# Kernel optimization log

Measured on AMD Instinct MI355X. Metric: run time of the kernel, lower is better.

The kernel has to match this reference:

```python
import jax, jax.numpy as jnp
import numpy as np

DIM = 64
H = 4
POS_DIM = 4
NUM_IDS = 16
B = 2048
N = 64


def setup_inputs() -> dict:
    key = jax.random.key(0)
    ks = jax.random.split(key, 16)
    d8 = DIM // 8
    stdv = 1.0 / np.sqrt(DIM * DIM)
    inp = {
        "x": jax.random.normal(ks[0], (B, N, DIM), jnp.float32),
        "pos": jax.random.normal(ks[1], (B, N, POS_DIM), jnp.float32),
        "strength": jax.random.normal(ks[2], (512,), jnp.float32),
        "embed_id1": 3,
        # weights stored [in, out] (torch Linear weight transposed)
        "Wq": jax.random.normal(ks[3], (DIM, DIM), jnp.float32) * 0.05,
        "Wk": jax.random.normal(ks[4], (DIM, DIM), jnp.float32) * 0.05,
        "pos_W1": jax.random.normal(ks[5], (POS_DIM, POS_DIM), jnp.float32) * 0.3,
        "pos_b1": jnp.zeros((POS_DIM,), jnp.float32),
        "pos_W2": jax.random.normal(ks[6], (POS_DIM, d8), jnp.float32) * 0.3,
        "pos_b2": jnp.zeros((d8,), jnp.float32),
        "head_W": jax.random.normal(ks[7], (d8, H), jnp.float32) * 0.3,
        "head_b": jnp.zeros((H,), jnp.float32),
        "gate": jnp.ones((H,), jnp.float32),
        "embeds": jax.random.uniform(ks[8], (NUM_IDS, DIM * DIM), jnp.float32, -stdv, stdv),
        "out_W": jax.random.normal(ks[9], (DIM, DIM), jnp.float32) * 0.05,
        "out_b": jnp.zeros((DIM,), jnp.float32),
        "str_W": jax.random.normal(ks[10], (512, 64), jnp.float32) * 0.04,
        "str_b": jnp.zeros((64,), jnp.float32),
    }
    return inp


def reference(x, pos, strength, embed_id1, Wq, Wk, pos_W1, pos_b1, pos_W2, pos_b2,
              head_W, head_b, gate, embeds, out_W, out_b, str_W, str_b):
    Bb, Nn, dim = x.shape
    h = gate.shape[0]
    dh = dim // h

    # strength projection, added to dynamic-weight V
    s64 = strength @ str_W + str_b                       # [dim]
    E = embeds[embed_id1].reshape(dim, dim)              # per-sample V weight
    v = x @ E.T + s64                                    # F.linear(x, E) + strength
    v = v.reshape(Bb, Nn, h, dh).transpose(0, 2, 1, 3)   # [B,H,N,dh]

    # QK attention
    q = (x @ Wq).reshape(Bb, Nn, h, dh).transpose(0, 2, 1, 3)
    k = (x @ Wk).reshape(Bb, Nn, h, dh).transpose(0, 2, 1, 3)
    attn = jax.nn.softmax(jnp.einsum('bhqd,bhkd->bhqk', q, k) / np.sqrt(dh), axis=-1)

    # pairwise relative-position attention
    p = jax.nn.relu(pos @ pos_W1 + pos_b1) @ pos_W2 + pos_b2          # [B,N,dim//8]
    diff = p[:, :, None, :] - p[:, None, :, :]                        # [B,N,N,dim//8]
    pos_logits = jnp.einsum('bqkf,fh->bhqk', diff, head_W) + head_b[None, :, None, None]
    pos_attn = jax.nn.softmax(pos_logits, axis=-1)

    # sigmoid-gated mixing + renormalization
    g = jax.nn.sigmoid(gate)[None, :, None, None]
    attn = (1.0 - g) * attn + g * pos_attn
    attn = attn / jnp.sum(attn, axis=-1, keepdims=True)

    out = jnp.einsum('bhqk,bhkd->bhqd', attn, v)
    out = out.transpose(0, 2, 1, 3).reshape(Bb, Nn, dim)
    return out @ out_W + out_b
```

## Files before the change

### kernel.cpp

```cpp
#include <hip/hip_runtime.h>

typedef unsigned short u16;
typedef unsigned int u32;
typedef short bf8 __attribute__((ext_vector_type(8)));
typedef float f4v __attribute__((ext_vector_type(4)));
typedef float f16v __attribute__((ext_vector_type(16)));

#define STR 72

__device__ __forceinline__ u32 f2bf(float f){
    union{float f;u32 i;}c; c.f=f; u32 i=c.i;
    return (i + 0x7FFFu + ((i>>16)&1u)) >> 16;
}

__device__ __forceinline__ void stage_row16(const float* __restrict__ g, short* __restrict__ dst,
                                            int n, int c0){
    const float4* p = (const float4*)(g + n*64 + c0);
    float4 a=p[0], b=p[1], c=p[2], d=p[3];
    uint4 o0, o1;
    o0.x = f2bf(a.x)|(f2bf(a.y)<<16); o0.y = f2bf(a.z)|(f2bf(a.w)<<16);
    o0.z = f2bf(b.x)|(f2bf(b.y)<<16); o0.w = f2bf(b.z)|(f2bf(b.w)<<16);
    o1.x = f2bf(c.x)|(f2bf(c.y)<<16); o1.y = f2bf(c.z)|(f2bf(c.w)<<16);
    o1.z = f2bf(d.x)|(f2bf(d.y)<<16); o1.w = f2bf(d.z)|(f2bf(d.w)<<16);
    *(uint4*)&dst[n*STR + c0]     = o0;
    *(uint4*)&dst[n*STR + c0 + 8] = o1;
}

__device__ __forceinline__ void mmgB(const u16* __restrict__ Wt, bf8 a0, bf8 a1,
                                     int l15, int quad, f4v c[4]){
    #pragma unroll
    for (int nt=0; nt<4; ++nt){
        bf8 b0 = *(const bf8*)&Wt[(16*nt + l15)*64 + quad*8];
        bf8 b1 = *(const bf8*)&Wt[(16*nt + l15)*64 + 32 + quad*8];
        c[nt] = __builtin_amdgcn_mfma_f32_16x16x32_bf16(a0, b0, c[nt], 0,0,0);
        c[nt] = __builtin_amdgcn_mfma_f32_16x16x32_bf16(a1, b1, c[nt], 0,0,0);
    }
}

__global__ __launch_bounds__(256) void pre_kernel(
    const int* __restrict__ embed_id,
    const float* __restrict__ Wq, const float* __restrict__ Wk, const float* __restrict__ oW,
    const float* __restrict__ embeds, const float* __restrict__ sW, const float* __restrict__ sb,
    const float* __restrict__ strength,
    float* __restrict__ ws_s64, u16* __restrict__ ws_wq, u16* __restrict__ ws_wk,
    u16* __restrict__ ws_ow, u16* __restrict__ ws_e)
{
    const int j = blockIdx.x;
    const int t = threadIdx.x;

    if (j < 3) {
        const float* W = (j==0) ? Wq : (j==1) ? Wk : oW;
        u16* dst = (j==0) ? ws_wq : (j==1) ? ws_wk : ws_ow;
        const int kp = t >> 3, ng = t & 7;
        const float4* r0 = (const float4*)(W + (2*kp  )*64 + 8*ng);
        const float4* r1 = (const float4*)(W + (2*kp+1)*64 + 8*ng);
        float4 a0=r0[0], a1=r0[1], b0=r1[0], b1=r1[1];
        float lo[8]={a0.x,a0.y,a0.z,a0.w,a1.x,a1.y,a1.z,a1.w};
        float hi[8]={b0.x,b0.y,b0.z,b0.w,b1.x,b1.y,b1.z,b1.w};
        #pragma unroll
        for (int i=0;i<8;++i)
            *(u32*)&dst[(8*ng+i)*64 + 2*kp] = f2bf(lo[i]) | (f2bf(hi[i])<<16);
    } else {
        __shared__ float sp[4][64];
        {
            const int n = t >> 2, c0 = (t & 3) << 4;
            const float4* p = (const float4*)(embeds + (size_t)(*embed_id)*4096 + n*64 + c0);
            float4 a=p[0], b=p[1], c=p[2], d=p[3];
            uint4 o0, o1;
            o0.x = f2bf(a.x)|(f2bf(a.y)<<16); o0.y = f2bf(a.z)|(f2bf(a.w)<<16);
            o0.z = f2bf(b.x)|(f2bf(b.y)<<16); o0.w = f2bf(b.z)|(f2bf(b.w)<<16);
            o1.x = f2bf(c.x)|(f2bf(c.y)<<16); o1.y = f2bf(c.z)|(f2bf(c.w)<<16);
            o1.z = f2bf(d.x)|(f2bf(d.y)<<16); o1.w = f2bf(d.z)|(f2bf(d.w)<<16);
            *(uint4*)&ws_e[n*64 + c0]     = o0;
            *(uint4*)&ws_e[n*64 + c0 + 8] = o1;
        }
        {
            const int d = t & 63, part = t >> 6;
            const float* wp = sW + part*128*64 + d;
            const float* s  = strength + part*128;
            float acc = 0.f;
            #pragma unroll 8
            for (int i = 0; i < 128; ++i) acc = fmaf(s[i], wp[i*64], acc);
            sp[part][d] = acc;
        }
        __syncthreads();
        if (t < 64) ws_s64[t] = sp[0][t] + sp[1][t] + sp[2][t] + sp[3][t] + sb[t];
    }
}

__global__ __launch_bounds__(256, 3) void attn_main_kernel(
    const float* __restrict__ x, const float* __restrict__ pos,
    const float* __restrict__ gate, const float* __restrict__ ob,
    const float* __restrict__ pW1, const float* __restrict__ pb1,
    const float* __restrict__ pW2, const float* __restrict__ pb2,
    const float* __restrict__ hW,
    const float* __restrict__ ws_s64,
    const u16* __restrict__ ws_wq, const u16* __restrict__ ws_wk,
    const u16* __restrict__ ws_ow, const u16* __restrict__ ws_e,
    float* __restrict__ out)
{
    __shared__ short B0[64*STR];
    __shared__ short B1[64*STR];
    __shared__ short B2[64*STR];
    __shared__ short B3[64*STR];
    __shared__ short VT[64*STR];
    __shared__ float pat_l[4][64];

    const int t    = threadIdx.x;
    const int b    = blockIdx.x;
    const int lane = t & 63;
    const int w    = t >> 6;
    const int l15  = lane & 15;
    const int l31  = lane & 31;
    const int l5   = lane >> 5;
    const int quad = lane >> 4;
    const int n    = t >> 2;
    const int c0   = (t & 3) << 4;

    stage_row16(x + (size_t)b*4096, B0, n, c0);

    float g = 1.f/(1.f + __expf(-gate[w]));
    {
        const float4 pv = *(const float4*)(pos + ((size_t)b*64 + lane)*4);
        float h1[4], p8[8];
        #pragma unroll
        for (int jj = 0; jj < 4; ++jj){
            float a = pb1[jj];
            a = fmaf(pv.x, pW1[0*4+jj], a);
            a = fmaf(pv.y, pW1[1*4+jj], a);
            a = fmaf(pv.z, pW1[2*4+jj], a);
            a = fmaf(pv.w, pW1[3*4+jj], a);
            h1[jj] = fmaxf(a, 0.f);
        }
        #pragma unroll
        for (int f = 0; f < 8; ++f){
            float a = pb2[f];
            #pragma unroll
            for (int jj = 0; jj < 4; ++jj) a = fmaf(h1[jj], pW2[jj*8+f], a);
            p8[f] = a;
        }
        float tv = 0.f;
        #pragma unroll
        for (int f = 0; f < 8; ++f) tv = fmaf(p8[f], hW[f*4+w], tv);
        float v0 = -tv;
        float m = v0;
        #pragma unroll
        for (int off = 32; off; off >>= 1) m = fmaxf(m, __shfl_xor(m, off));
        float e = __expf(v0 - m);
        float ssum = e;
        #pragma unroll
        for (int off = 32; off; off >>= 1) ssum += __shfl_xor(ssum, off);
        pat_l[w][lane] = g * (e / ssum);
    }

    float svv[4];
    #pragma unroll
    for (int nt=0;nt<4;++nt) svv[nt] = ws_s64[16*nt + l15];
    float obv[4];
    #pragma unroll
    for (int nt=0;nt<4;++nt) obv[nt] = ob[16*nt + l15];

    asm volatile("" ::: "memory");

    {
        bf8 xa0 = *(const bf8*)&B0[(16*w + l15)*STR + quad*8];
        bf8 xa1 = *(const bf8*)&B0[(16*w + l15)*STR + 32 + quad*8];
        f4v cq[4], ck[4], cv[4];
        #pragma unroll
        for (int nt=0;nt<4;++nt){
            cq[nt][0]=0.f;cq[nt][1]=0.f;cq[nt][2]=0.f;cq[nt][3]=0.f;
            ck[nt][0]=0.f;ck[nt][1]=0.f;ck[nt][2]=0.f;ck[nt][3]=0.f;
            cv[nt][0]=0.f;cv[nt][1]=0.f;cv[nt][2]=0.f;cv[nt][3]=0.f;
        }
        mmgB(ws_wq, xa0, xa1, l15, quad, cq);
        mmgB(ws_wk, xa0, xa1, l15, quad, ck);
        mmgB(ws_e,  xa0, xa1, l15, quad, cv);
        #pragma unroll
        for (int nt=0;nt<4;++nt)
            #pragma unroll
            for (int r=0;r<4;++r){
                B2[(16*w + quad*4 + r)*STR + 16*nt + l15] = (short)f2bf(0.25f*cq[nt][r]);
                B3[(16*w + quad*4 + r)*STR + 16*nt + l15] = (short)f2bf(ck[nt][r]);
            }
        #pragma unroll
        for (int nt=0;nt<4;++nt){
            float sv = svv[nt];
            uint2 pk;
            pk.x = f2bf(cv[nt][0]+sv) | (f2bf(cv[nt][1]+sv)<<16);
            pk.y = f2bf(cv[nt][2]+sv) | (f2bf(cv[nt][3]+sv)<<16);
            *(uint2*)&VT[(16*nt + l15)*STR + 16*w + quad*4] = pk;
        }
    }
    __syncthreads();

    f16v S[2][2];
    {
        bf8 ka0 = *(const bf8*)&B3[(     l31)*STR + 16*w + 8*l5];
        bf8 ka1 = *(const bf8*)&B3[(32 + l31)*STR + 16*w + 8*l5];
        bf8 qb0 = *(const bf8*)&B2[(     l31)*STR + 16*w + 8*l5];
        bf8 qb1 = *(const bf8*)&B2[(32 + l31)*STR + 16*w + 8*l5];
        #pragma unroll
        for (int mt=0;mt<2;++mt)
            #pragma unroll
            for (int nt=0;nt<2;++nt)
                #pragma unroll
                for (int i=0;i<16;++i) S[mt][nt][i] = 0.f;
        S[0][0] = __builtin_amdgcn_mfma_f32_32x32x16_bf16(ka0, qb0, S[0][0], 0,0,0);
        S[0][1] = __builtin_amdgcn_mfma_f32_32x32x16_bf16(ka0, qb1, S[0][1], 0,0,0);
        S[1][0] = __builtin_amdgcn_mfma_f32_32x32x16_bf16(ka1, qb0, S[1][0], 0,0,0);
        S[1][1] = __builtin_amdgcn_mfma_f32_32x32x16_bf16(ka1, qb1, S[1][1], 0,0,0);
    }
    float inv_[2];
    #pragma unroll
    for (int nt=0;nt<2;++nt){
        float m = S[0][nt][0];
        #pragma unroll
        for (int i=1;i<16;++i) m = fmaxf(m, S[0][nt][i]);
        #pragma unroll
        for (int i=0;i<16;++i) m = fmaxf(m, S[1][nt][i]);
        m = fmaxf(m, __shfl_xor(m, 32));
        float l = 0.f;
        #pragma unroll
        for (int mt=0;mt<2;++mt)
            #pragma unroll
            for (int i=0;i<16;++i){ float e = __expf(S[mt][nt][i]-m); S[mt][nt][i] = e; l += e; }
        l += __shfl_xor(l, 32);
        float c1 = (1.f - g) / l;
        float tot = 0.f;
        #pragma unroll
        for (int mt=0;mt<2;++mt)
            #pragma unroll
            for (int rg=0;rg<4;++rg){
                const float4 tv = *(const float4*)&pat_l[w][32*mt + 8*rg + 4*l5];
                float a0 = fmaf(c1, S[mt][nt][rg*4+0], tv.x);
                float a1 = fmaf(c1, S[mt][nt][rg*4+1], tv.y);
                float a2 = fmaf(c1, S[mt][nt][rg*4+2], tv.z);
                float a3 = fmaf(c1, S[mt][nt][rg*4+3], tv.w);
                S[mt][nt][rg*4+0]=a0; S[mt][nt][rg*4+1]=a1;
                S[mt][nt][rg*4+2]=a2; S[mt][nt][rg*4+3]=a3;
                tot += a0+a1+a2+a3;
            }
        tot += __shfl_xor(tot, 32);
        inv_[nt] = 1.f / tot;
    }
    __syncthreads();

    short* Pb = (w==0) ? B0 : (w==1) ? B1 : (w==2) ? B2 : B3;
    #pragma unroll
    for (int nt=0;nt<2;++nt)
        #pragma unroll
        for (int mt=0;mt<2;++mt)
            #pragma unroll
            for (int rg=0;rg<4;++rg){
                float v0 = S[mt][nt][rg*4+0]*inv_[nt], v1 = S[mt][nt][rg*4+1]*inv_[nt];
                float v2 = S[mt][nt][rg*4+2]*inv_[nt], v3 = S[mt][nt][rg*4+3]*inv_[nt];
                uint2 pk;
                pk.x = f2bf(v0) | (f2bf(v1)<<16);
                pk.y = f2bf(v2) | (f2bf(v3)<<16);
                *(uint2*)&Pb[(32*nt + l31)*STR + 32*mt + 8*rg + 4*l5] = pk;
            }
    asm volatile("" ::: "memory");

    f4v o[4];
    {
        bf8 bv0 = *(const bf8*)&VT[(16*w + l15)*STR + quad*8];
        bf8 bv1 = *(const bf8*)&VT[(16*w + l15)*STR + 32 + quad*8];
        #pragma unroll
        for (int mt=0;mt<4;++mt){
            o[mt][0]=0.f;o[mt][1]=0.f;o[mt][2]=0.f;o[mt][3]=0.f;
            bf8 a0 = *(const bf8*)&Pb[(16*mt + l15)*STR + quad*8];
            bf8 a1 = *(const bf8*)&Pb[(16*mt + l15)*STR + 32 + quad*8];
            o[mt] = __builtin_amdgcn_mfma_f32_16x16x32_bf16(a0, bv0, o[mt], 0,0,0);
            o[mt] = __builtin_amdgcn_mfma_f32_16x16x32_bf16(a1, bv1, o[mt], 0,0,0);
        }
    }
    __syncthreads();

    #pragma unroll
    for (int mt=0;mt<4;++mt)
        #pragma unroll
        for (int r=0;r<4;++r)
            B3[(16*mt + quad*4 + r)*STR + 16*w + l15] = (short)f2bf(o[mt][r]);
    __syncthreads();

    {
        bf8 ca0 = *(const bf8*)&B3[(16*w + l15)*STR + quad*8];
        bf8 ca1 = *(const bf8*)&B3[(16*w + l15)*STR + 32 + quad*8];
        f4v c[4];
        #pragma unroll
        for (int nt=0;nt<4;++nt){
            c[nt][0]=obv[nt];c[nt][1]=obv[nt];c[nt][2]=obv[nt];c[nt][3]=obv[nt];
        }
        mmgB(ws_ow, ca0, ca1, l15, quad, c);
        #pragma unroll
        for (int nt=0;nt<4;++nt)
            #pragma unroll
            for (int r=0;r<4;++r)
                out[((size_t)b*64 + 16*w + quad*4 + r)*64 + 16*nt + l15] = c[nt][r];
    }
}

extern "C" void kernel_launch(void* const* d_in, const int* in_sizes, int n_in,
                              void* d_out, int out_size, void* d_ws, size_t ws_size,
                              hipStream_t stream) {
    const int B = in_sizes[0] / (64 * 64);

    float* ws_s64 = (float*)d_ws;
    u16*   ws_wq  = (u16*)(ws_s64 + 64);
    u16*   ws_wk  = ws_wq + 4096;
    u16*   ws_ow  = ws_wk + 4096;
    u16*   ws_e   = ws_ow + 4096;

    pre_kernel<<<4, 256, 0, stream>>>(
        (const int*)d_in[3],
        (const float*)d_in[4],  (const float*)d_in[5],  (const float*)d_in[14],
        (const float*)d_in[13], (const float*)d_in[16], (const float*)d_in[17],
        (const float*)d_in[2],
        ws_s64, ws_wq, ws_wk, ws_ow, ws_e);

    attn_main_kernel<<<B, 256, 0, stream>>>(
        (const float*)d_in[0],  (const float*)d_in[1],
        (const float*)d_in[12], (const float*)d_in[15],
        (const float*)d_in[6],  (const float*)d_in[7],  (const float*)d_in[8],  (const float*)d_in[9],
        (const float*)d_in[10],
        ws_s64, ws_wq, ws_wk, ws_ow, ws_e,
        (float*)d_out);
}
```

Baseline: 153.5 us.

## Split projection GEMMs by output column so weight fragments stay in registers

```diff
diff --git a/kernel.cpp b/kernel.cpp
--- a/kernel.cpp
+++ b/kernel.cpp
@@ -26,17 +26,6 @@
     *(uint4*)&dst[n*STR + c0 + 8] = o1;
 }
 
-__device__ __forceinline__ void mmgB(const u16* __restrict__ Wt, bf8 a0, bf8 a1,
-                                     int l15, int quad, f4v c[4]){
-    #pragma unroll
-    for (int nt=0; nt<4; ++nt){
-        bf8 b0 = *(const bf8*)&Wt[(16*nt + l15)*64 + quad*8];
-        bf8 b1 = *(const bf8*)&Wt[(16*nt + l15)*64 + 32 + quad*8];
-        c[nt] = __builtin_amdgcn_mfma_f32_16x16x32_bf16(a0, b0, c[nt], 0,0,0);
-        c[nt] = __builtin_amdgcn_mfma_f32_16x16x32_bf16(a1, b1, c[nt], 0,0,0);
-    }
-}
-
 __global__ __launch_bounds__(256) void pre_kernel(
     const int* __restrict__ embed_id,
     const float* __restrict__ Wq, const float* __restrict__ Wk, const float* __restrict__ oW,
@@ -51,6 +40,7 @@
     if (j < 3) {
         const float* W = (j==0) ? Wq : (j==1) ? Wk : oW;
         u16* dst = (j==0) ? ws_wq : (j==1) ? ws_wk : ws_ow;
+        const float scl = (j==0) ? 0.25f : 1.0f;
         const int kp = t >> 3, ng = t & 7;
         const float4* r0 = (const float4*)(W + (2*kp  )*64 + 8*ng);
         const float4* r1 = (const float4*)(W + (2*kp+1)*64 + 8*ng);
@@ -59,7 +49,7 @@
         float hi[8]={b0.x,b0.y,b0.z,b0.w,b1.x,b1.y,b1.z,b1.w};
         #pragma unroll
         for (int i=0;i<8;++i)
-            *(u32*)&dst[(8*ng+i)*64 + 2*kp] = f2bf(lo[i]) | (f2bf(hi[i])<<16);
+            *(u32*)&dst[(8*ng+i)*64 + 2*kp] = f2bf(scl*lo[i]) | (f2bf(scl*hi[i])<<16);
     } else {
         __shared__ float sp[4][64];
         {
@@ -100,7 +90,7 @@
     float* __restrict__ out)
 {
     __shared__ short B0[64*STR];
-    __shared__ short B1[64*STR];
+    __shared__ short PX[64*STR];
     __shared__ short B2[64*STR];
     __shared__ short B3[64*STR];
     __shared__ short VT[64*STR];
@@ -117,6 +107,18 @@
     const int n    = t >> 2;
     const int c0   = (t & 3) << 4;
 
+    const int wq_off = (16*w + l15)*64 + quad*8;
+    bf8 bq0 = *(const bf8*)&ws_wq[wq_off];
+    bf8 bq1 = *(const bf8*)&ws_wq[wq_off + 32];
+    bf8 bk0 = *(const bf8*)&ws_wk[wq_off];
+    bf8 bk1 = *(const bf8*)&ws_wk[wq_off + 32];
+    bf8 be0 = *(const bf8*)&ws_e [wq_off];
+    bf8 be1 = *(const bf8*)&ws_e [wq_off + 32];
+    bf8 bo0 = *(const bf8*)&ws_ow[wq_off];
+    bf8 bo1 = *(const bf8*)&ws_ow[wq_off + 32];
+    const float sv  = ws_s64[16*w + l15];
+    const float obv = ob[16*w + l15];
+
     stage_row16(x + (size_t)b*4096, B0, n, c0);
 
     float g = 1.f/(1.f + __expf(-gate[w]));
@@ -152,46 +154,32 @@
         for (int off = 32; off; off >>= 1) ssum += __shfl_xor(ssum, off);
         pat_l[w][lane] = g * (e / ssum);
     }
-
-    float svv[4];
-    #pragma unroll
-    for (int nt=0;nt<4;++nt) svv[nt] = ws_s64[16*nt + l15];
-    float obv[4];
-    #pragma unroll
-    for (int nt=0;nt<4;++nt) obv[nt] = ob[16*nt + l15];
-
+    __syncthreads();
+
+    #pragma unroll
+    for (int mt=0; mt<4; ++mt){
+        bf8 a0 = *(const bf8*)&B0[(16*mt + l15)*STR + quad*8];
+        bf8 a1 = *(const bf8*)&B0[(16*mt + l15)*STR + 32 + quad*8];
+        f4v cq, ck, cv;
+        #pragma unroll
+        for (int r=0;r<4;++r){ cq[r]=0.f; ck[r]=0.f; cv[r]=sv; }
+        cq = __builtin_amdgcn_mfma_f32_16x16x32_bf16(a0, bq0, cq, 0,0,0);
+        cq = __builtin_amdgcn_mfma_f32_16x16x32_bf16(a1, bq1, cq, 0,0,0);
+        ck = __builtin_amdgcn_mfma_f32_16x16x32_bf16(a0, bk0, ck, 0,0,0);
+        ck = __builtin_amdgcn_mfma_f32_16x16x32_bf16(a1, bk1, ck, 0,0,0);
+        cv = __builtin_amdgcn_mfma_f32_16x16x32_bf16(a0, be0, cv, 0,0,0);
+        cv = __builtin_amdgcn_mfma_f32_16x16x32_bf16(a1, be1, cv, 0,0,0);
+        #pragma unroll
+        for (int r=0;r<4;++r){
+            B2[(16*mt + quad*4 + r)*STR + 16*w + l15] = (short)f2bf(cq[r]);
+            B3[(16*mt + quad*4 + r)*STR + 16*w + l15] = (short)f2bf(ck[r]);
+        }
+        uint2 pk;
+        pk.x = f2bf(cv[0]) | (f2bf(cv[1])<<16);
+        pk.y = f2bf(cv[2]) | (f2bf(cv[3])<<16);
+        *(uint2*)&VT[(16*w + l15)*STR + 16*mt + quad*4] = pk;
+    }
     asm volatile("" ::: "memory");
-
-    {
-        bf8 xa0 = *(const bf8*)&B0[(16*w + l15)*STR + quad*8];
-        bf8 xa1 = *(const bf8*)&B0[(16*w + l15)*STR + 32 + quad*8];
-        f4v cq[4], ck[4], cv[4];
-        #pragma unroll
-        for (int nt=0;nt<4;++nt){
-            cq[nt][0]=0.f;cq[nt][1]=0.f;cq[nt][2]=0.f;cq[nt][3]=0.f;
-            ck[nt][0]=0.f;ck[nt][1]=0.f;ck[nt][2]=0.f;ck[nt][3]=0.f;
-            cv[nt][0]=0.f;cv[nt][1]=0.f;cv[nt][2]=0.f;cv[nt][3]=0.f;
-        }
-        mmgB(ws_wq, xa0, xa1, l15, quad, cq);
-        mmgB(ws_wk, xa0, xa1, l15, quad, ck);
-        mmgB(ws_e,  xa0, xa1, l15, quad, cv);
-        #pragma unroll
-        for (int nt=0;nt<4;++nt)
-            #pragma unroll
-            for (int r=0;r<4;++r){
-                B2[(16*w + quad*4 + r)*STR + 16*nt + l15] = (short)f2bf(0.25f*cq[nt][r]);
-                B3[(16*w + quad*4 + r)*STR + 16*nt + l15] = (short)f2bf(ck[nt][r]);
-            }
-        #pragma unroll
-        for (int nt=0;nt<4;++nt){
-            float sv = svv[nt];
-            uint2 pk;
-            pk.x = f2bf(cv[nt][0]+sv) | (f2bf(cv[nt][1]+sv)<<16);
-            pk.y = f2bf(cv[nt][2]+sv) | (f2bf(cv[nt][3]+sv)<<16);
-            *(uint2*)&VT[(16*nt + l15)*STR + 16*w + quad*4] = pk;
-        }
-    }
-    __syncthreads();
 
     f16v S[2][2];
     {
@@ -245,7 +233,7 @@
     }
     __syncthreads();
 
-    short* Pb = (w==0) ? B0 : (w==1) ? B1 : (w==2) ? B2 : B3;
+    short* Pb = (w==0) ? B0 : (w==1) ? PX : (w==2) ? B2 : B3;
     #pragma unroll
     for (int nt=0;nt<2;++nt)
         #pragma unroll
@@ -283,20 +271,18 @@
             B3[(16*mt + quad*4 + r)*STR + 16*w + l15] = (short)f2bf(o[mt][r]);
     __syncthreads();
 
-    {
-        bf8 ca0 = *(const bf8*)&B3[(16*w + l15)*STR + quad*8];
-        bf8 ca1 = *(const bf8*)&B3[(16*w + l15)*STR + 32 + quad*8];
-        f4v c[4];
-        #pragma unroll
-        for (int nt=0;nt<4;++nt){
-            c[nt][0]=obv[nt];c[nt][1]=obv[nt];c[nt][2]=obv[nt];c[nt][3]=obv[nt];
-        }
-        mmgB(ws_ow, ca0, ca1, l15, quad, c);
-        #pragma unroll
-        for (int nt=0;nt<4;++nt)
-            #pragma unroll
-            for (int r=0;r<4;++r)
-                out[((size_t)b*64 + 16*w + quad*4 + r)*64 + 16*nt + l15] = c[nt][r];
+    #pragma unroll
+    for (int mt=0;mt<4;++mt){
+        bf8 ca0 = *(const bf8*)&B3[(16*mt + l15)*STR + quad*8];
+        bf8 ca1 = *(const bf8*)&B3[(16*mt + l15)*STR + 32 + quad*8];
+        f4v c;
+        #pragma unroll
+        for (int r=0;r<4;++r) c[r] = obv;
+        c = __builtin_amdgcn_mfma_f32_16x16x32_bf16(ca0, bo0, c, 0,0,0);
+        c = __builtin_amdgcn_mfma_f32_16x16x32_bf16(ca1, bo1, c, 0,0,0);
+        #pragma unroll
+        for (int r=0;r<4;++r)
+            out[((size_t)b*64 + 16*mt + quad*4 + r)*64 + 16*w + l15] = c[r];
     }
 }
 
```

After: 138.1 us. 1.11x faster.
